# Kernel tuning notes

Hardware: AMD Instinct MI355X
Metric: run time of the kernel (lower is better)

Reference implementation:

```python
import jax, jax.numpy as jnp
import numpy as np
import math

N, E, O, C, KD, KEYD = 50000, 800000, 4, 64, 16, 128


def setup_inputs() -> dict:
    key = jax.random.key(0)
    ks = jax.random.split(key, 10)
    x = jax.random.normal(ks[0], (N, O, C), jnp.float32)
    kernel_basis = jax.random.normal(ks[1], (E, O, KD), jnp.float32)
    fiber_kernel_basis = jax.random.normal(ks[2], (O, O, KD), jnp.float32)
    edge_index = jax.random.randint(ks[3], (2, E), 0, N, jnp.int32)
    # nn.Linear default init ~ U(-1/sqrt(fan_in), 1/sqrt(fan_in)); scaled normal is fine as data
    kernel_W = jax.random.normal(ks[4], (C, KD), jnp.float32) / math.sqrt(KD)        # kernel: Linear(kernel_dim -> in_channels)
    fiber_kernel_W = jax.random.normal(ks[5], (C, KD), jnp.float32) / math.sqrt(KD)  # depthwise: in*out/groups = C
    key_W = jax.random.normal(ks[6], (KEYD, C), jnp.float32) / math.sqrt(C)
    key_b = jnp.zeros((KEYD,), jnp.float32)
    query_W = jax.random.normal(ks[7], (KEYD, C), jnp.float32) / math.sqrt(C)
    query_b = jnp.zeros((KEYD,), jnp.float32)
    bias = jnp.zeros((C,), jnp.float32)
    return {"x": x, "kernel_basis": kernel_basis, "fiber_kernel_basis": fiber_kernel_basis,
            "edge_index": edge_index, "kernel_W": kernel_W, "fiber_kernel_W": fiber_kernel_W,
            "key_W": key_W, "key_b": key_b, "query_W": query_W, "query_b": query_b, "bias": bias}


def reference(x, kernel_basis, fiber_kernel_basis, edge_index, kernel_W, fiber_kernel_W,
              key_W, key_b, query_W, query_b, bias):
    src = edge_index[0]
    dst = edge_index[1]
    n = x.shape[0]
    # per-edge spatial kernel: [E,O,KD] @ [KD,C] -> [E,O,C]
    k = jnp.einsum('eok,ck->eoc', kernel_basis, kernel_W)
    message = x[src] * k                                       # [E,O,C]
    # scatter-softmax attention over incoming edges of each target node
    keys = jnp.einsum('noc,kc->nok', x, key_W) + key_b        # [N,O,KEYD]
    queries = jnp.einsum('noc,kc->nok', x, query_W) + query_b
    logits = jnp.sum(keys[src] * queries[dst], axis=-1, keepdims=True) / math.sqrt(KEYD)  # [E,O,1]
    e = jnp.exp(logits - jnp.max(logits))                      # global-max stabilization, as in source
    denom = jax.ops.segment_sum(e, dst, num_segments=n) + 1e-6 # [N,O,1]
    att = e / denom[dst]
    message = message * att
    # scatter-add aggregation into target nodes
    x1 = jax.ops.segment_sum(message, dst, num_segments=n)     # [N,O,C]
    # fiber (orientation) mixing kernel: [O,O,KD] @ [KD,C] -> [O,O,C]
    fk = jnp.einsum('pok,ck->poc', fiber_kernel_basis, fiber_kernel_W)
    x2 = jnp.einsum('boc,poc->bpc', x1, fk) / fk.shape[-2]
    return x2 + bias
```

## Files before the change

kernel.cpp:

```cpp
#include <hip/hip_runtime.h>
#include <math.h>

#define NN 50000
#define EE 800000
#define OO 4
#define CC 64
#define KDD 16
#define KEYDD 128
#define CH 16

typedef float v2f __attribute__((ext_vector_type(2)));

__device__ __forceinline__ float wave_red_sum(float v) {
  int x;
  x = __builtin_amdgcn_update_dpp(0, __float_as_int(v), 0x111, 0xf, 0xf, false);
  v += __int_as_float(x);
  x = __builtin_amdgcn_update_dpp(0, __float_as_int(v), 0x112, 0xf, 0xf, false);
  v += __int_as_float(x);
  x = __builtin_amdgcn_update_dpp(0, __float_as_int(v), 0x114, 0xf, 0xf, false);
  v += __int_as_float(x);
  x = __builtin_amdgcn_update_dpp(0, __float_as_int(v), 0x118, 0xf, 0xf, false);
  v += __int_as_float(x);
  x = __builtin_amdgcn_update_dpp(0, __float_as_int(v), 0x142, 0xa, 0xf, false);
  v += __int_as_float(x);
  x = __builtin_amdgcn_update_dpp(0, __float_as_int(v), 0x143, 0xc, 0xf, false);
  v += __int_as_float(x);
  return __int_as_float(__builtin_amdgcn_readlane(__float_as_int(v), 63));
}

__device__ __forceinline__ float exp2_fast(float x) {
  float r;
  asm("v_exp_f32 %0, %1" : "=v"(r) : "v"(x));
  return r;
}

__device__ __forceinline__ void red4(float q0, float q1, float q2, float q3,
                                     float& p0, float& p1, float& p2, float& p3) {
  asm("s_nop 1\n\tv_permlane32_swap_b32 %0, %1" : "+v"(q0), "+v"(q1));
  float ra = q0 + q1;
  asm("s_nop 1\n\tv_permlane32_swap_b32 %0, %1" : "+v"(q2), "+v"(q3));
  float rb = q2 + q3;
  asm("s_nop 1\n\t"
      "v_add_f32_dpp %0, %0, %0 row_shr:1 row_mask:0xf bank_mask:0xf bound_ctrl:0\n\t"
      "v_add_f32_dpp %1, %1, %1 row_shr:1 row_mask:0xf bank_mask:0xf bound_ctrl:0\n\t"
      "v_add_f32_dpp %0, %0, %0 row_shr:2 row_mask:0xf bank_mask:0xf bound_ctrl:0\n\t"
      "v_add_f32_dpp %1, %1, %1 row_shr:2 row_mask:0xf bank_mask:0xf bound_ctrl:0\n\t"
      "v_add_f32_dpp %0, %0, %0 row_shr:4 row_mask:0xf bank_mask:0xf bound_ctrl:0\n\t"
      "v_add_f32_dpp %1, %1, %1 row_shr:4 row_mask:0xf bank_mask:0xf bound_ctrl:0\n\t"
      "v_add_f32_dpp %0, %0, %0 row_shr:8 row_mask:0xf bank_mask:0xf bound_ctrl:0\n\t"
      "v_add_f32_dpp %1, %1, %1 row_shr:8 row_mask:0xf bank_mask:0xf bound_ctrl:0\n\t"
      "v_add_f32_dpp %0, %0, %0 row_bcast:15 row_mask:0xa bank_mask:0xf bound_ctrl:0\n\t"
      "v_add_f32_dpp %1, %1, %1 row_bcast:15 row_mask:0xa bank_mask:0xf bound_ctrl:0\n\t"
      "s_nop 0"
      : "+v"(ra), "+v"(rb));
  p0 = __int_as_float(__builtin_amdgcn_readlane(__float_as_int(ra), 31));
  p1 = __int_as_float(__builtin_amdgcn_readlane(__float_as_int(ra), 63));
  p2 = __int_as_float(__builtin_amdgcn_readlane(__float_as_int(rb), 31));
  p3 = __int_as_float(__builtin_amdgcn_readlane(__float_as_int(rb), 63));
}

__global__ void prep_kernel(const float* __restrict__ keyW, const float* __restrict__ keyB,
                            const float* __restrict__ qryW, const float* __restrict__ qryB,
                            const float* __restrict__ fkb, const float* __restrict__ fkw,
                            float* __restrict__ Mt, float* __restrict__ aVec,
                            float* __restrict__ bVec, float* __restrict__ c0,
                            float* __restrict__ fk) {
  __shared__ float qw[KEYDD * CC];
  __shared__ float kws[KEYDD * 4];
  int t = threadIdx.x, b = blockIdx.x;
  if (b < 16) {
    for (int i = t; i < KEYDD * CC; i += 256) qw[i] = qryW[i];
    for (int i = t; i < KEYDD * 4; i += 256) {
      int k = i >> 2, c1l = i & 3;
      kws[i] = keyW[k * CC + b * 4 + c1l];
    }
    __syncthreads();
    int c1l = t >> 6, c2 = t & 63;
    float s = 0.f;
    #pragma unroll 8
    for (int k = 0; k < KEYDD; ++k)
      s = fmaf(kws[k * 4 + c1l], qw[k * CC + c2], s);
    Mt[c2 * CC + b * 4 + c1l] = s;
  } else {
    if (t < CC) {
      float sa = 0.f, sb = 0.f;
      for (int k = 0; k < KEYDD; ++k) {
        sa = fmaf(keyB[k], qryW[k * CC + t], sa);
        sb = fmaf(qryB[k], keyW[k * CC + t], sb);
      }
      aVec[t] = sa; bVec[t] = sb;
    }
    if (t == 0) {
      float s = 0.f;
      for (int k = 0; k < KEYDD; ++k) s = fmaf(keyB[k], qryB[k], s);
      c0[0] = s;
    }
    for (int idx = t; idx < OO * OO * CC; idx += 256) {
      int p = idx >> 8, rem = idx & 255;
      int o = rem >> 6, c = rem & 63;
      float s = 0.f;
      #pragma unroll
      for (int kd = 0; kd < KDD; ++kd)
        s = fmaf(fkb[(p * OO + o) * KDD + kd], fkw[c * KDD + kd], s);
      fk[idx] = 0.25f * s;
    }
  }
}

__global__ void count_kernel(const int* __restrict__ ei, int* __restrict__ counts) {
  int e = blockIdx.x * 256 + threadIdx.x;
  if (e < EE) atomicAdd(&counts[ei[EE + e]], 1);
}

__global__ void scan1_kernel(const int* __restrict__ counts, int* __restrict__ incl,
                             int* __restrict__ bsum, int n) {
  __shared__ int buf[256];
  int t = threadIdx.x;
  int i = blockIdx.x * 256 + t;
  int v = (i < n) ? counts[i] : 0;
  buf[t] = v;
  __syncthreads();
  for (int off = 1; off < 256; off <<= 1) {
    int a = buf[t];
    int b2 = (t >= off) ? buf[t - off] : 0;
    __syncthreads();
    buf[t] = a + b2;
    __syncthreads();
  }
  if (i < n) incl[i] = buf[t];
  if (t == 255) bsum[blockIdx.x] = buf[255];
}
__global__ void scan2_kernel(const int* __restrict__ bsum, int* __restrict__ bbase, int nb) {
  __shared__ int buf[256];
  int t = threadIdx.x;
  int v = (t < nb) ? bsum[t] : 0;
  buf[t] = v;
  __syncthreads();
  for (int off = 1; off < 256; off <<= 1) {
    int a = buf[t];
    int b2 = (t >= off) ? buf[t - off] : 0;
    __syncthreads();
    buf[t] = a + b2;
    __syncthreads();
  }
  if (t < nb) bbase[t] = buf[t] - v;
}
__global__ void scan3_kernel(const int* __restrict__ counts, const int* __restrict__ incl,
                             const int* __restrict__ bbase, int* __restrict__ offsets, int n) {
  int i = blockIdx.x * 256 + threadIdx.x;
  if (i < n) {
    int oi = bbase[blockIdx.x] + incl[i];
    offsets[i] = oi - counts[i];
    if (i == n - 1) offsets[n] = oi;
  }
}

__global__ void fill_kernel(const int* __restrict__ ei, const int* __restrict__ offsets,
                            int* __restrict__ counts, long long* __restrict__ pairs) {
  int e = blockIdx.x * 256 + threadIdx.x;
  if (e < EE) {
    int d = ei[EE + e];
    int r = atomicSub(&counts[d], 1) - 1;
    int pos = offsets[d] + r;
    pairs[pos] = ((long long)ei[e] << 32) | (unsigned)e;
  }
}

__device__ __forceinline__ float kv_dot(const float* __restrict__ kb, int ej, int obase,
                                        float4 kw0, float4 kw1, float4 kw2, float4 kw3) {
  const float4* bp = reinterpret_cast<const float4*>(kb + ej * (OO * KDD) + obase);
  float4 b0 = bp[0], b1 = bp[1], b2 = bp[2], b3 = bp[3];
  v2f a0 = {0.f, 0.f}, a1 = {0.f, 0.f};
  #define P2(f4, i) (reinterpret_cast<const v2f*>(&(f4))[i])
  a0 = __builtin_elementwise_fma(P2(b0, 0), P2(kw0, 0), a0);
  a1 = __builtin_elementwise_fma(P2(b0, 1), P2(kw0, 1), a1);
  a0 = __builtin_elementwise_fma(P2(b1, 0), P2(kw1, 0), a0);
  a1 = __builtin_elementwise_fma(P2(b1, 1), P2(kw1, 1), a1);
  a0 = __builtin_elementwise_fma(P2(b2, 0), P2(kw2, 0), a0);
  a1 = __builtin_elementwise_fma(P2(b2, 1), P2(kw2, 1), a1);
  a0 = __builtin_elementwise_fma(P2(b3, 0), P2(kw3, 0), a0);
  a1 = __builtin_elementwise_fma(P2(b3, 1), P2(kw3, 1), a1);
  #undef P2
  v2f s = a0 + a1;
  return s.x + s.y;
}

__global__ __launch_bounds__(256, 4) void mega_kernel(
    const float* __restrict__ x, const float* __restrict__ Mt,
    const float* __restrict__ aVec, const float* __restrict__ bVec,
    const float* __restrict__ c0p, const float* __restrict__ kb,
    const float* __restrict__ kW, const int* __restrict__ offsets,
    const long long* __restrict__ pairs, const float* __restrict__ fkg,
    const float* __restrict__ bias, float* __restrict__ out) {
  __shared__ float xs[OO * CC];
  __shared__ float x1[OO * CC];
  int n = blockIdx.x;
  int t = threadIdx.x;
  int o = __builtin_amdgcn_readfirstlane(t >> 6);
  int c = t & 63;
  const float scale2 = 0.12751541050862828f;
  int js = offsets[n], je = offsets[n + 1];
  int deg = je - js;

  float xown = x[(size_t)n * (OO * CC) + t];
  xs[t] = xown;
  __syncthreads();

  int lane16 = c & 15;
  long long pr = 0;
  if (deg > 0) pr = pairs[js + min(lane16, deg - 1)];

  float ubr = 0.f;
  #pragma unroll 8
  for (int c2 = 0; c2 < CC; ++c2)
    ubr = fmaf(Mt[c2 * CC + c], xs[o * CC + c2], ubr);
  ubr += bVec[c];
  float base2 = (wave_red_sum(aVec[c] * xown) + c0p[0]) * scale2;

  const float4* kwp = reinterpret_cast<const float4*>(kW + c * KDD);
  float4 kw0 = kwp[0], kw1 = kwp[1], kw2 = kwp[2], kw3 = kwp[3];
  int obase = o * KDD;

  float m2 = -INFINITY, S = 0.f, acc = 0.f;

  for (int cs = 0; cs < deg; cs += CH) {
    int cl = deg - cs; if (cl > CH) cl = CH;
    int e_v = (int)((unsigned long long)pr & 0xffffffffu);
    int s_v = (int)(pr >> 32);
    float xv[CH];
    #pragma unroll
    for (int j = 0; j < CH; ++j) {
      int sj = __builtin_amdgcn_readlane(s_v, j);
      xv[j] = x[(size_t)(sj * OO + o) * CC + c];
    }
    int ns = cs + CH;
    if (ns < deg) {
      int ncl = deg - ns;
      pr = pairs[js + ns + min(lane16, ncl - 1)];
    }
    #define SUB4(J0)                                                           \
    {                                                                          \
      float kv0 = kv_dot(kb, __builtin_amdgcn_readlane(e_v, (J0) + 0), obase, kw0, kw1, kw2, kw3); \
      float kv1 = kv_dot(kb, __builtin_amdgcn_readlane(e_v, (J0) + 1), obase, kw0, kw1, kw2, kw3); \
      float kv2 = kv_dot(kb, __builtin_amdgcn_readlane(e_v, (J0) + 2), obase, kw0, kw1, kw2, kw3); \
      float kv3 = kv_dot(kb, __builtin_amdgcn_readlane(e_v, (J0) + 3), obase, kw0, kw1, kw2, kw3); \
      float p0, p1, p2, p3;                                                    \
      red4(xv[(J0) + 0] * ubr, xv[(J0) + 1] * ubr,                             \
           xv[(J0) + 2] * ubr, xv[(J0) + 3] * ubr, p0, p1, p2, p3);            \
      float l0 = ((J0) + 0 < cl) ? fmaf(p0, scale2, base2) : -INFINITY;        \
      float l1 = ((J0) + 1 < cl) ? fmaf(p1, scale2, base2) : -INFINITY;        \
      float l2 = ((J0) + 2 < cl) ? fmaf(p2, scale2, base2) : -INFINITY;        \
      float l3 = ((J0) + 3 < cl) ? fmaf(p3, scale2, base2) : -INFINITY;        \
      float cm = fmaxf(fmaxf(l0, l1), fmaxf(l2, l3));                          \
      if (cm > m2) {                                                           \
        float rsc = exp2_fast(m2 - cm);                                        \
        S *= rsc; acc *= rsc; m2 = cm;                                         \
      }                                                                        \
      float ev0 = exp2_fast(l0 - m2);                                          \
      float ev1 = exp2_fast(l1 - m2);                                          \
      float ev2 = exp2_fast(l2 - m2);                                          \
      float ev3 = exp2_fast(l3 - m2);                                          \
      S += (ev0 + ev1) + (ev2 + ev3);                                          \
      acc = fmaf(ev0 * kv0, xv[(J0) + 0], acc);                                \
      acc = fmaf(ev1 * kv1, xv[(J0) + 1], acc);                                \
      acc = fmaf(ev2 * kv2, xv[(J0) + 2], acc);                                \
      acc = fmaf(ev3 * kv3, xv[(J0) + 3], acc);                                \
    }
    SUB4(0)
    if (cl > 4)  SUB4(4)
    if (cl > 8)  SUB4(8)
    if (cl > 12) SUB4(12)
    #undef SUB4
  }

  float invd = 1.0f / (S + 1e-6f);
  x1[t] = acc * invd;
  __syncthreads();
  float s2s = 0.f;
  #pragma unroll
  for (int oo = 0; oo < OO; ++oo)
    s2s = fmaf(x1[oo * CC + c], fkg[o * (OO * CC) + oo * CC + c], s2s);
  out[(size_t)n * (OO * CC) + t] = s2s + bias[c];
}

extern "C" void kernel_launch(void* const* d_in, const int* in_sizes, int n_in,
                              void* d_out, int out_size, void* d_ws, size_t ws_size,
                              hipStream_t stream) {
  const float* x    = (const float*)d_in[0];
  const float* kb   = (const float*)d_in[1];
  const float* fkb  = (const float*)d_in[2];
  const int*   ei   = (const int*)d_in[3];
  const float* kW   = (const float*)d_in[4];
  const float* fkW  = (const float*)d_in[5];
  const float* keyW = (const float*)d_in[6];
  const float* keyB = (const float*)d_in[7];
  const float* qryW = (const float*)d_in[8];
  const float* qryB = (const float*)d_in[9];
  const float* bias = (const float*)d_in[10];
  float* out = (float*)d_out;

  const int NB = (NN + 255) / 256;

  float* wsf  = (float*)d_ws;
  float* Mt   = wsf;
  float* aVec = Mt + 4096;
  float* bVec = aVec + 64;
  float* c0   = bVec + 64;
  float* fk   = c0 + 64;
  long long* pairs = (long long*)(fk + 1024);
  int* counts    = (int*)(pairs + EE);
  int* offsets   = counts + NN;
  int* incl      = offsets + NN + 1;
  int* bsum      = incl + NN;
  int* bbase     = bsum + 256;

  hipMemsetAsync(counts, 0, (size_t)NN * sizeof(int), stream);

  prep_kernel<<<17, 256, 0, stream>>>(keyW, keyB, qryW, qryB, fkb, fkW, Mt, aVec, bVec, c0, fk);
  count_kernel<<<(EE + 255) / 256, 256, 0, stream>>>(ei, counts);
  scan1_kernel<<<NB, 256, 0, stream>>>(counts, incl, bsum, NN);
  scan2_kernel<<<1, 256, 0, stream>>>(bsum, bbase, NB);
  scan3_kernel<<<NB, 256, 0, stream>>>(counts, incl, bbase, offsets, NN);
  fill_kernel<<<(EE + 255) / 256, 256, 0, stream>>>(ei, offsets, counts, pairs);
  mega_kernel<<<NN, 256, 0, stream>>>(x, Mt, aVec, bVec, c0, kb, kW, offsets, pairs,
                                      fk, bias, out);
}
```

Measured before the change: 420.6 us.

## Drop online-softmax max tracking and batch-load up to 64 edge pairs per wave

Removes the running-max rescaling from the per-node softmax. Logits are taken relative to the node's own constant base, which is folded into the epsilon term of the denominator, so the branch and rescale work per 4-edge group go away. Edge (index, source) pairs are now loaded 64 lanes at a time up front, replacing the per-chunk prefetch of 16, and the scale is folded into ubr. The risk is overflow in exp2 without max subtraction if logits minus base are large, since the global-max stabilization no longer has an analogue.

```diff
diff --git a/kernel.cpp b/kernel.cpp
--- a/kernel.cpp
+++ b/kernel.cpp
@@ -206,60 +206,57 @@
   xs[t] = xown;
   __syncthreads();
 
-  int lane16 = c & 15;
   long long pr = 0;
-  if (deg > 0) pr = pairs[js + min(lane16, deg - 1)];
+  if (deg > 0) pr = pairs[js + min(c, deg - 1)];
 
   float ubr = 0.f;
   #pragma unroll 8
   for (int c2 = 0; c2 < CC; ++c2)
     ubr = fmaf(Mt[c2 * CC + c], xs[o * CC + c2], ubr);
-  ubr += bVec[c];
+  ubr = (ubr + bVec[c]) * scale2;
   float base2 = (wave_red_sum(aVec[c] * xown) + c0p[0]) * scale2;
 
   const float4* kwp = reinterpret_cast<const float4*>(kW + c * KDD);
   float4 kw0 = kwp[0], kw1 = kwp[1], kw2 = kwp[2], kw3 = kwp[3];
   int obase = o * KDD;
 
-  float m2 = -INFINITY, S = 0.f, acc = 0.f;
+  int e_v = (int)((unsigned long long)pr & 0xffffffffu);
+  int s_v = (int)(pr >> 32);
+  float S = 0.f, acc = 0.f;
+  int lane16 = c & 15;
 
   for (int cs = 0; cs < deg; cs += CH) {
     int cl = deg - cs; if (cl > CH) cl = CH;
-    int e_v = (int)((unsigned long long)pr & 0xffffffffu);
-    int s_v = (int)(pr >> 32);
+    int eW = e_v, sW = s_v, lo0 = cs;
+    if (cs >= 64) {
+      long long pr2 = pairs[js + cs + min(lane16, cl - 1)];
+      eW = (int)((unsigned long long)pr2 & 0xffffffffu);
+      sW = (int)(pr2 >> 32);
+      lo0 = 0;
+    }
     float xv[CH];
     #pragma unroll
     for (int j = 0; j < CH; ++j) {
-      int sj = __builtin_amdgcn_readlane(s_v, j);
+      int sj = __builtin_amdgcn_readlane(sW, lo0 + j);
       xv[j] = x[(size_t)(sj * OO + o) * CC + c];
-    }
-    int ns = cs + CH;
-    if (ns < deg) {
-      int ncl = deg - ns;
-      pr = pairs[js + ns + min(lane16, ncl - 1)];
     }
     #define SUB4(J0)                                                           \
     {                                                                          \
-      float kv0 = kv_dot(kb, __builtin_amdgcn_readlane(e_v, (J0) + 0), obase, kw0, kw1, kw2, kw3); \
-      float kv1 = kv_dot(kb, __builtin_amdgcn_readlane(e_v, (J0) + 1), obase, kw0, kw1, kw2, kw3); \
-      float kv2 = kv_dot(kb, __builtin_amdgcn_readlane(e_v, (J0) + 2), obase, kw0, kw1, kw2, kw3); \
-      float kv3 = kv_dot(kb, __builtin_amdgcn_readlane(e_v, (J0) + 3), obase, kw0, kw1, kw2, kw3); \
+      float kv0 = kv_dot(kb, __builtin_amdgcn_readlane(eW, lo0 + (J0) + 0), obase, kw0, kw1, kw2, kw3); \
+      float kv1 = kv_dot(kb, __builtin_amdgcn_readlane(eW, lo0 + (J0) + 1), obase, kw0, kw1, kw2, kw3); \
+      float kv2 = kv_dot(kb, __builtin_amdgcn_readlane(eW, lo0 + (J0) + 2), obase, kw0, kw1, kw2, kw3); \
+      float kv3 = kv_dot(kb, __builtin_amdgcn_readlane(eW, lo0 + (J0) + 3), obase, kw0, kw1, kw2, kw3); \
       float p0, p1, p2, p3;                                                    \
       red4(xv[(J0) + 0] * ubr, xv[(J0) + 1] * ubr,                             \
            xv[(J0) + 2] * ubr, xv[(J0) + 3] * ubr, p0, p1, p2, p3);            \
-      float l0 = ((J0) + 0 < cl) ? fmaf(p0, scale2, base2) : -INFINITY;        \
-      float l1 = ((J0) + 1 < cl) ? fmaf(p1, scale2, base2) : -INFINITY;        \
-      float l2 = ((J0) + 2 < cl) ? fmaf(p2, scale2, base2) : -INFINITY;        \
-      float l3 = ((J0) + 3 < cl) ? fmaf(p3, scale2, base2) : -INFINITY;        \
-      float cm = fmaxf(fmaxf(l0, l1), fmaxf(l2, l3));                          \
-      if (cm > m2) {                                                           \
-        float rsc = exp2_fast(m2 - cm);                                        \
-        S *= rsc; acc *= rsc; m2 = cm;                                         \
-      }                                                                        \
-      float ev0 = exp2_fast(l0 - m2);                                          \
-      float ev1 = exp2_fast(l1 - m2);                                          \
-      float ev2 = exp2_fast(l2 - m2);                                          \
-      float ev3 = exp2_fast(l3 - m2);                                          \
+      float l0 = ((J0) + 0 < cl) ? p0 : -INFINITY;                             \
+      float l1 = ((J0) + 1 < cl) ? p1 : -INFINITY;                             \
+      float l2 = ((J0) + 2 < cl) ? p2 : -INFINITY;                             \
+      float l3 = ((J0) + 3 < cl) ? p3 : -INFINITY;                             \
+      float ev0 = exp2_fast(l0);                                               \
+      float ev1 = exp2_fast(l1);                                               \
+      float ev2 = exp2_fast(l2);                                               \
+      float ev3 = exp2_fast(l3);                                               \
       S += (ev0 + ev1) + (ev2 + ev3);                                          \
       acc = fmaf(ev0 * kv0, xv[(J0) + 0], acc);                                \
       acc = fmaf(ev1 * kv1, xv[(J0) + 1], acc);                                \
@@ -273,7 +270,7 @@
     #undef SUB4
   }
 
-  float invd = 1.0f / (S + 1e-6f);
+  float invd = 1.0f / (S + 1e-6f * exp2_fast(-base2));
   x1[t] = acc * invd;
   __syncthreads();
   float s2s = 0.f;
```

After: 485.9 us. +15.5%, slower.
